# Kernel optimization log

Hardware: AMD Instinct MI355X
Metric: run time of the kernel (lower is better)

## Reference

```python
import jax, jax.numpy as jnp
import numpy as np

N = 20000        # nodes
E = 320000       # edges (avg degree 16)
NHID = 256       # hidden dim (decoder input features)
NFEAT = 256      # reconstructed attribute dim
K_SELECTED = 4096  # number of nodes with label == 1 (static for jit)


def setup_inputs() -> dict:
    key = jax.random.key(0)
    ks = jax.random.split(key, 12)
    feature_attribute = jax.random.normal(ks[0], (N, NHID), dtype=jnp.float32)
    edge_row = jax.random.randint(ks[1], (E,), 0, N, dtype=jnp.int32)
    edge_col = jax.random.randint(ks[2], (E,), 0, N, dtype=jnp.int32)
    # positive, roughly degree-normalized adjacency weights
    edge_w = jax.random.uniform(ks[3], (E,), dtype=jnp.float32) / 16.0
    # first K_SELECTED nodes are labeled 1, rest 0 (static count for jit)
    labels = jnp.concatenate([jnp.ones((K_SELECTED,), jnp.int32),
                              jnp.zeros((N - K_SELECTED,), jnp.int32)])
    stdv1 = 1.0 / np.sqrt(NHID)
    stdv2 = 1.0 / np.sqrt(NFEAT)
    W1_ad = jax.random.uniform(ks[4], (NHID, NHID), minval=-stdv1, maxval=stdv1, dtype=jnp.float32)
    b1_ad = jax.random.uniform(ks[5], (NHID,), minval=-stdv1, maxval=stdv1, dtype=jnp.float32)
    W2_ad = jax.random.uniform(ks[6], (NHID, NFEAT), minval=-stdv2, maxval=stdv2, dtype=jnp.float32)
    b2_ad = jax.random.uniform(ks[7], (NFEAT,), minval=-stdv2, maxval=stdv2, dtype=jnp.float32)
    W_sd = jax.random.uniform(ks[8], (NHID, NHID), minval=-stdv1, maxval=stdv1, dtype=jnp.float32)
    b_sd = jax.random.uniform(ks[9], (NHID,), minval=-stdv1, maxval=stdv1, dtype=jnp.float32)
    return dict(feature_attribute=feature_attribute, edge_row=edge_row, edge_col=edge_col,
                edge_w=edge_w, labels=labels, W1_ad=W1_ad, b1_ad=b1_ad,
                W2_ad=W2_ad, b2_ad=b2_ad, W_sd=W_sd, b_sd=b_sd)


def reference(feature_attribute, edge_row, edge_col, edge_w, labels,
              W1_ad, b1_ad, W2_ad, b2_ad, W_sd, b_sd):
    def gcn(x, W, b):
        support = x @ W                                   # [N, d_out] dense mm
        msg = support[edge_col] * edge_w[:, None]         # gather + scale [E, d_out]
        out = jax.ops.segment_sum(msg, edge_row, num_segments=N)  # spmm aggregation
        return out + b

    # static-size index of labeled nodes (labels==1 count is K_SELECTED)
    idx = jnp.nonzero(labels == 1, size=K_SELECTED)[0]

    # Attribute decoder: relu(gc1) -> (dropout, eval: identity) -> gc2 -> select
    h = jax.nn.relu(gcn(feature_attribute, W1_ad, b1_ad))
    pred_attribute_mat = gcn(h, W2_ad, b2_ad)[idx]        # [K, NFEAT]

    # Structure decoder: gc1 -> select -> x @ x.T
    s = gcn(feature_attribute, W_sd, b_sd)[idx]           # [K, NHID]
    pred_adj_mat = s @ s.T                                # [K, K]

    return pred_attribute_mat, pred_adj_mat
```

## Files before the change

### kernel.cpp

```cpp
#include <hip/hip_runtime.h>
#include <hip/hip_bf16.h>

#define NN   20000
#define NE   320000
#define KSEL 4096

typedef short bf16x8 __attribute__((ext_vector_type(8)));
typedef float f32x4  __attribute__((ext_vector_type(4)));

static __device__ __forceinline__ float bf2f(unsigned short u){
  return __uint_as_float(((unsigned int)u) << 16);
}
static __device__ __forceinline__ unsigned short f2bf(float f){
  unsigned int x = __float_as_uint(f);
  x += 0x7fffu + ((x >> 16) & 1u);
  return (unsigned short)(x >> 16);
}
static __device__ __forceinline__ void gld_lds16(const unsigned short* g, unsigned short* l){
  __builtin_amdgcn_global_load_lds(
      (const __attribute__((address_space(1))) unsigned int*)g,
      (__attribute__((address_space(3))) unsigned int*)l, 16, 0, 0);
}

__global__ __launch_bounds__(256) void k_prep0(const float* __restrict__ W1,
    const float* __restrict__ Wsd, const float* __restrict__ W2,
    const int* __restrict__ labels,
    unsigned short* __restrict__ Wt, int* __restrict__ counts, int* __restrict__ partA){
  int b = blockIdx.x, tid = threadIdx.x;
  if (b < 48){
    __shared__ unsigned short lt[64 * 65];
    int w = b >> 4, t = b & 15;
    int tR = (t >> 2) * 64, tC = (t & 3) * 64;
    const float* W = (w == 0) ? W1 : (w == 1 ? Wsd : W2);
    #pragma unroll
    for (int it = 0; it < 16; ++it){
      int lin = it * 256 + tid;
      int r = lin >> 6, c = lin & 63;
      lt[c * 65 + r] = f2bf(W[(size_t)(tR + r) * 256 + tC + c]);
    }
    __syncthreads();
    #pragma unroll
    for (int it = 0; it < 16; ++it){
      int lin = it * 256 + tid;
      int o = lin >> 6, k = lin & 63;
      Wt[(size_t)w * 65536 + (size_t)(tC + o) * 256 + tR + k] = lt[o * 65 + k];
    }
  } else {
    __shared__ int ws[4];
    int z = b - 48, lane = tid & 63, wv = tid >> 6;
    if (tid < 250) *(int4*)&counts[z * 1000 + tid * 4] = make_int4(0, 0, 0, 0);
    int base = z * 1024 + tid * 4;
    int s = 0;
    #pragma unroll
    for (int j = 0; j < 4; ++j){
      int n0 = base + j;
      if (n0 < NN) s += (labels[n0] == 1) ? 1 : 0;
    }
    #pragma unroll
    for (int off = 32; off; off >>= 1) s += __shfl_down(s, off, 64);
    if (lane == 0) ws[wv] = s;
    __syncthreads();
    if (tid == 0) partA[z] = ws[0] + ws[1] + ws[2] + ws[3];
  }
}

__global__ __launch_bounds__(256) void k_main1(const float* __restrict__ X,
    const int* __restrict__ row, const int* __restrict__ labels,
    const int* __restrict__ partA,
    unsigned short* __restrict__ Xb, int* __restrict__ counts, int* __restrict__ idx){
  int b = blockIdx.x, tid = threadIdx.x;
  if (b < 2500){
    int i = (b * 256 + tid) * 8;
    float4 v0 = *(const float4*)(X + i);
    float4 v1 = *(const float4*)(X + i + 4);
    bf16x8 o;
    o[0] = (short)f2bf(v0.x); o[1] = (short)f2bf(v0.y);
    o[2] = (short)f2bf(v0.z); o[3] = (short)f2bf(v0.w);
    o[4] = (short)f2bf(v1.x); o[5] = (short)f2bf(v1.y);
    o[6] = (short)f2bf(v1.z); o[7] = (short)f2bf(v1.w);
    *(bf16x8*)(Xb + i) = o;
  } else if (b < 3750){
    int e = (b - 2500) * 256 + tid;
    atomicAdd(&counts[row[e]], 1);
  } else {
    __shared__ int ws[4];
    __shared__ int boff_s;
    int bx = b - 3750;
    int lane = tid & 63, wv = tid >> 6;
    if (tid < 64){
      int v = (lane < 20) ? partA[lane] : 0;
      int acc = v;
      #pragma unroll
      for (int off = 1; off < 32; off <<= 1){
        int t = __shfl_up(acc, off, 64);
        if (lane >= off) acc += t;
      }
      if (lane == bx) boff_s = acc - v;
    }
    int base = bx * 1024 + tid * 4;
    int c[4]; int s = 0;
    #pragma unroll
    for (int j = 0; j < 4; ++j){
      int n0 = base + j;
      c[j] = (n0 < NN && labels[n0] == 1) ? 1 : 0;
      s += c[j];
    }
    int incl = s;
    #pragma unroll
    for (int off = 1; off < 64; off <<= 1){
      int t = __shfl_up(incl, off, 64);
      if (lane >= off) incl += t;
    }
    if (lane == 63) ws[wv] = incl;
    __syncthreads();
    int woff = boff_s;
    for (int w = 0; w < wv; ++w) woff += ws[w];
    int off = woff + incl - s;
    #pragma unroll
    for (int j = 0; j < 4; ++j){
      if (c[j]){ if (off < KSEL) idx[off] = base + j; ++off; }
    }
  }
}

__global__ __launch_bounds__(256) void k_row_emit(const int* __restrict__ counts,
    int* __restrict__ start, int* __restrict__ cursor){
  __shared__ int ws[4];
  __shared__ int red[4];
  int tid = threadIdx.x, lane = tid & 63, wv = tid >> 6;
  int base = blockIdx.x * 1024;
  int ps = 0;
  for (int i = tid * 4; i < base; i += 1024){
    int4 v = *(const int4*)&counts[i];
    ps += v.x + v.y + v.z + v.w;
  }
  #pragma unroll
  for (int off = 32; off; off >>= 1) ps += __shfl_down(ps, off, 64);
  if (lane == 0) red[wv] = ps;
  __syncthreads();
  int bpref = red[0] + red[1] + red[2] + red[3];
  int nb = base + tid * 4;
  int c[4]; int s = 0;
  #pragma unroll
  for (int j = 0; j < 4; ++j){
    int n0 = nb + j;
    c[j] = (n0 < NN) ? counts[n0] : 0;
    s += c[j];
  }
  int incl = s;
  #pragma unroll
  for (int off = 1; off < 64; off <<= 1){
    int t = __shfl_up(incl, off, 64);
    if (lane >= off) incl += t;
  }
  if (lane == 63) ws[wv] = incl;
  __syncthreads();
  int woff = bpref;
  for (int w = 0; w < wv; ++w) woff += ws[w];
  int run = woff + incl - s;
  #pragma unroll
  for (int j = 0; j < 4; ++j){
    int n0 = nb + j;
    if (n0 < NN){ start[n0] = run; cursor[n0] = run; run += c[j]; }
  }
  if (blockIdx.x == 0 && tid == 0) start[NN] = NE;
}

__global__ void k_scatter(const int* __restrict__ row, const int* __restrict__ col,
                          const float* __restrict__ ew, int* __restrict__ cursor,
                          int2* __restrict__ rec){
  int e = blockIdx.x * 256 + threadIdx.x;
  if (e < NE){
    int r = row[e];
    int p = atomicAdd(&cursor[r], 1);
    rec[p] = make_int2(col[e], __float_as_int(ew[e]));
  }
}

__global__ __launch_bounds__(256) void k_spmm_full(const unsigned short* __restrict__ Xb,
    const int* __restrict__ start, const int2* __restrict__ rec,
    unsigned short* __restrict__ aggX){
  int wave = threadIdx.x >> 6, lane = threadIdx.x & 63;
  int half = lane >> 5, hl = lane & 31;
  int n = blockIdx.x * 4 + wave;
  int s = start[n], e = start[n + 1];
  int d = hl * 8;
  float acc[8] = {};
  for (int base = s; base < e; base += 64){
    int p = base + lane;
    int pc = p < e ? p : e - 1;
    int2 r = rec[pc];
    float wv = (p < e) ? __int_as_float(r.y) : 0.0f;
    int m = e - base; if (m > 64) m = 64;
    for (int j = 0; j < m; j += 8){
      int j0 = j + half, j1 = j + 2 + half, j2 = j + 4 + half, j3 = j + 6 + half;
      int   c0 = __shfl(r.x, j0), c1 = __shfl(r.x, j1);
      int   c2 = __shfl(r.x, j2), c3 = __shfl(r.x, j3);
      float w0 = __shfl(wv, j0),  w1 = __shfl(wv, j1);
      float w2 = __shfl(wv, j2),  w3 = __shfl(wv, j3);
      bf16x8 v0 = *(const bf16x8*)&Xb[(size_t)c0 * 256 + d];
      bf16x8 v1 = *(const bf16x8*)&Xb[(size_t)c1 * 256 + d];
      bf16x8 v2 = *(const bf16x8*)&Xb[(size_t)c2 * 256 + d];
      bf16x8 v3 = *(const bf16x8*)&Xb[(size_t)c3 * 256 + d];
      #pragma unroll
      for (int q = 0; q < 8; ++q){
        acc[q] += w0 * bf2f((unsigned short)v0[q]) + w1 * bf2f((unsigned short)v1[q])
                + w2 * bf2f((unsigned short)v2[q]) + w3 * bf2f((unsigned short)v3[q]);
      }
    }
  }
  #pragma unroll
  for (int q = 0; q < 8; ++q){
    float o = __shfl(acc[q], hl + 32);
    acc[q] += o;
  }
  if (half == 0){
    bf16x8 ob;
    #pragma unroll
    for (int q = 0; q < 8; ++q) ob[q] = (short)f2bf(acc[q]);
    *(bf16x8*)&aggX[(size_t)n * 256 + d] = ob;
  }
}

__global__ __launch_bounds__(256) void k_gemm_h(const unsigned short* __restrict__ A,
                                                const unsigned short* __restrict__ Wt,
                                                const float* __restrict__ bias,
                                                unsigned short* __restrict__ out, int M){
  __shared__ unsigned short At[128 * 64];
  __shared__ unsigned short Bt[64 * 64];
  int tid = threadIdx.x, wave = tid >> 6, lane = tid & 63;
  int lm = lane & 15, lq = lane >> 4;
  int mBase = blockIdx.x * 128;
  int oBase = blockIdx.y * 64;
  f32x4 acc[2][4] = {};
  for (int kc = 0; kc < 256; kc += 64){
    if (kc) __syncthreads();
    #pragma unroll
    for (int it = 0; it < 4; ++it){
      int s = (wave * 4 + it) * 64 + lane;
      int row = s >> 3, c = (s & 7) ^ (row & 7);
      int gr = mBase + row; if (gr >= M) gr = M - 1;
      gld_lds16(&A[(size_t)gr * 256 + kc + c * 8], &At[s * 8]);
    }
    #pragma unroll
    for (int it = 0; it < 2; ++it){
      int s = (wave * 2 + it) * 64 + lane;
      int row = s >> 3, c = (s & 7) ^ (row & 7);
      gld_lds16(&Wt[(size_t)(oBase + row) * 256 + kc + c * 8], &Bt[s * 8]);
    }
    __syncthreads();
    #pragma unroll
    for (int ks = 0; ks < 64; ks += 32){
      int cb = ks >> 3;
      int RA = wave * 32 + lm;
      int ca = ((cb + lq) ^ (RA & 7)) << 3;
      bf16x8 a0 = *(const bf16x8*)&At[RA * 64 + ca];
      bf16x8 a1 = *(const bf16x8*)&At[(RA + 16) * 64 + ca];
      #pragma unroll
      for (int os = 0; os < 4; ++os){
        int RB = os * 16 + lm;
        bf16x8 b = *(const bf16x8*)&Bt[RB * 64 + (((cb + lq) ^ (RB & 7)) << 3)];
        acc[0][os] = __builtin_amdgcn_mfma_f32_16x16x32_bf16(a0, b, acc[0][os], 0, 0, 0);
        acc[1][os] = __builtin_amdgcn_mfma_f32_16x16x32_bf16(a1, b, acc[1][os], 0, 0, 0);
      }
    }
  }
  #pragma unroll
  for (int ms = 0; ms < 2; ++ms){
    int rb = mBase + wave * 32 + ms * 16 + lq * 4;
    #pragma unroll
    for (int os = 0; os < 4; ++os){
      int col = oBase + os * 16 + lm;
      float bv = bias[col];
      #pragma unroll
      for (int r = 0; r < 4; ++r){
        int row = rb + r;
        if (row < M) out[(size_t)row * 256 + col] = f2bf(fmaxf(acc[ms][os][r] + bv, 0.f));
      }
    }
  }
}

__global__ __launch_bounds__(256) void k_tail1(const unsigned short* __restrict__ h,
    const int* __restrict__ idx, const int* __restrict__ start, const int2* __restrict__ rec,
    unsigned short* __restrict__ aggH, const unsigned short* __restrict__ aggX,
    const unsigned short* __restrict__ Wt, const float* __restrict__ bsd,
    unsigned short* __restrict__ sel){
  int tid = threadIdx.x, wave = tid >> 6, lane = tid & 63;
  if (blockIdx.x < 128){
    int lm = lane & 15, lq = lane >> 4;
    int b2 = blockIdx.x;
    int mBase = (b2 & 31) * 128, oBase = (b2 >> 5) * 64;
    const unsigned short* W = Wt + 256 * 256;
    int r0 = mBase + wave * 32 + lm;
    const unsigned short* A0 = aggX + (size_t)idx[r0] * 256;
    const unsigned short* A1 = aggX + (size_t)idx[r0 + 16] * 256;
    f32x4 acc[2][4] = {};
    #pragma unroll
    for (int ks = 0; ks < 256; ks += 32){
      int ka = ks + lq * 8;
      bf16x8 a0 = *(const bf16x8*)&A0[ka];
      bf16x8 a1 = *(const bf16x8*)&A1[ka];
      #pragma unroll
      for (int os = 0; os < 4; ++os){
        bf16x8 b = *(const bf16x8*)&W[(size_t)(oBase + os * 16 + lm) * 256 + ka];
        acc[0][os] = __builtin_amdgcn_mfma_f32_16x16x32_bf16(a0, b, acc[0][os], 0, 0, 0);
        acc[1][os] = __builtin_amdgcn_mfma_f32_16x16x32_bf16(a1, b, acc[1][os], 0, 0, 0);
      }
    }
    #pragma unroll
    for (int ms = 0; ms < 2; ++ms){
      int rb = mBase + wave * 32 + ms * 16 + lq * 4;
      #pragma unroll
      for (int os = 0; os < 4; ++os){
        int col = oBase + os * 16 + lm;
        float bv = bsd[col];
        #pragma unroll
        for (int r = 0; r < 4; ++r)
          sel[(size_t)(rb + r) * 256 + col] = f2bf(acc[ms][os][r] + bv);
      }
    }
    return;
  }
  int half = lane >> 5, hl = lane & 31;
  int i = (blockIdx.x - 128) * 4 + wave;
  int n = idx[i];
  int s = start[n], e = start[n + 1];
  int d = hl * 8;
  float acc[8] = {};
  for (int base = s; base < e; base += 64){
    int p = base + lane;
    int pc = p < e ? p : e - 1;
    int2 r = rec[pc];
    float wv = (p < e) ? __int_as_float(r.y) : 0.0f;
    int m = e - base; if (m > 64) m = 64;
    for (int j = 0; j < m; j += 8){
      int j0 = j + half, j1 = j + 2 + half, j2 = j + 4 + half, j3 = j + 6 + half;
      int   c0 = __shfl(r.x, j0), c1 = __shfl(r.x, j1);
      int   c2 = __shfl(r.x, j2), c3 = __shfl(r.x, j3);
      float w0 = __shfl(wv, j0),  w1 = __shfl(wv, j1);
      float w2 = __shfl(wv, j2),  w3 = __shfl(wv, j3);
      bf16x8 v0 = *(const bf16x8*)&h[(size_t)c0 * 256 + d];
      bf16x8 v1 = *(const bf16x8*)&h[(size_t)c1 * 256 + d];
      bf16x8 v2 = *(const bf16x8*)&h[(size_t)c2 * 256 + d];
      bf16x8 v3 = *(const bf16x8*)&h[(size_t)c3 * 256 + d];
      #pragma unroll
      for (int q = 0; q < 8; ++q){
        acc[q] += w0 * bf2f((unsigned short)v0[q]) + w1 * bf2f((unsigned short)v1[q])
                + w2 * bf2f((unsigned short)v2[q]) + w3 * bf2f((unsigned short)v3[q]);
      }
    }
  }
  #pragma unroll
  for (int q = 0; q < 8; ++q){
    float o = __shfl(acc[q], hl + 32);
    acc[q] += o;
  }
  if (half == 0){
    bf16x8 ob;
    #pragma unroll
    for (int q = 0; q < 8; ++q) ob[q] = (short)f2bf(acc[q]);
    *(bf16x8*)&aggH[(size_t)i * 256 + d] = ob;
  }
}

__global__ __launch_bounds__(256) void k_tail2(const unsigned short* __restrict__ aggH,
    const unsigned short* __restrict__ Wt, const float* __restrict__ b2v,
    float* __restrict__ out0, const unsigned short* __restrict__ S,
    float* __restrict__ out1){
  __shared__ __align__(16) char smem[34816];
  int tid = threadIdx.x, wave = tid >> 6, lane = tid & 63;
  int lm = lane & 15, lq = lane >> 4;
  if (blockIdx.x < 128){
    int b2 = blockIdx.x;
    int mBase = (b2 & 31) * 128, oBase = (b2 >> 5) * 64;
    const unsigned short* W = Wt + 512 * 256;
    const unsigned short* A0 = aggH + (size_t)(mBase + wave * 32 + lm) * 256;
    const unsigned short* A1 = A0 + 16 * 256;
    f32x4 acc[2][4] = {};
    #pragma unroll
    for (int ks = 0; ks < 256; ks += 32){
      int ka = ks + lq * 8;
      bf16x8 a0 = *(const bf16x8*)&A0[ka];
      bf16x8 a1 = *(const bf16x8*)&A1[ka];
      #pragma unroll
      for (int os = 0; os < 4; ++os){
        bf16x8 b = *(const bf16x8*)&W[(size_t)(oBase + os * 16 + lm) * 256 + ka];
        acc[0][os] = __builtin_amdgcn_mfma_f32_16x16x32_bf16(a0, b, acc[0][os], 0, 0, 0);
        acc[1][os] = __builtin_amdgcn_mfma_f32_16x16x32_bf16(a1, b, acc[1][os], 0, 0, 0);
      }
    }
    #pragma unroll
    for (int ms = 0; ms < 2; ++ms){
      int rb = mBase + wave * 32 + ms * 16 + lq * 4;
      #pragma unroll
      for (int os = 0; os < 4; ++os){
        int col = oBase + os * 16 + lm;
        float bv = b2v[col];
        #pragma unroll
        for (int r = 0; r < 4; ++r)
          out0[(size_t)(rb + r) * 256 + col] = acc[ms][os][r] + bv;
      }
    }
    return;
  }
  int t = blockIdx.x - 128;
  int bx = (int)((sqrtf(8.f * (float)t + 1.f) - 1.f) * 0.5f);
  while ((bx + 1) * (bx + 2) / 2 <= t) ++bx;
  while (bx * (bx + 1) / 2 > t) --bx;
  int by = t - bx * (bx + 1) / 2;
  int mBase = bx * 128, oBase = by * 128;
  unsigned short* At = (unsigned short*)smem;
  unsigned short* Bt = (unsigned short*)(smem + 16384);
  f32x4 acc[2][8] = {};
  for (int kc = 0; kc < 256; kc += 64){
    if (kc) __syncthreads();
    #pragma unroll
    for (int it = 0; it < 4; ++it){
      int s = (wave * 4 + it) * 64 + lane;
      int row = s >> 3, c = (s & 7) ^ (row & 7);
      gld_lds16(&S[(size_t)(mBase + row) * 256 + kc + c * 8], &At[s * 8]);
      gld_lds16(&S[(size_t)(oBase + row) * 256 + kc + c * 8], &Bt[s * 8]);
    }
    __syncthreads();
    #pragma unroll
    for (int ks = 0; ks < 64; ks += 32){
      int cb = ks >> 3;
      int RA = wave * 32 + lm;
      int ca = ((cb + lq) ^ (RA & 7)) << 3;
      bf16x8 a0 = *(const bf16x8*)&At[RA * 64 + ca];
      bf16x8 a1 = *(const bf16x8*)&At[(RA + 16) * 64 + ca];
      #pragma unroll
      for (int os = 0; os < 8; ++os){
        int RB = os * 16 + lm;
        bf16x8 b = *(const bf16x8*)&Bt[RB * 64 + (((cb + lq) ^ (RB & 7)) << 3)];
        acc[0][os] = __builtin_amdgcn_mfma_f32_16x16x32_bf16(a0, b, acc[0][os], 0, 0, 0);
        acc[1][os] = __builtin_amdgcn_mfma_f32_16x16x32_bf16(a1, b, acc[1][os], 0, 0, 0);
      }
    }
  }
  #pragma unroll
  for (int ms = 0; ms < 2; ++ms){
    int rb = mBase + wave * 32 + ms * 16 + lq * 4;
    #pragma unroll
    for (int os = 0; os < 8; ++os){
      int col = oBase + os * 16 + lm;
      #pragma unroll
      for (int r = 0; r < 4; ++r)
        out1[(size_t)(rb + r) * 4096 + col] = acc[ms][os][r];
    }
  }
  if (bx == by) return;
  float* fst = (float*)smem;
  #pragma unroll
  for (int half = 0; half < 2; ++half){
    __syncthreads();
    #pragma unroll
    for (int ms = 0; ms < 2; ++ms){
      int mr = wave * 32 + ms * 16 + lq * 4;
      #pragma unroll
      for (int os2 = 0; os2 < 4; ++os2){
        int oc = os2 * 16 + lm;
        *(f32x4*)&fst[oc * 136 + mr] = acc[ms][half * 4 + os2];
      }
    }
    __syncthreads();
    int l = tid & 31, ocb = tid >> 5;
    #pragma unroll
    for (int it = 0; it < 8; ++it){
      int oc = it * 8 + ocb;
      f32x4 v = *(const f32x4*)&fst[oc * 136 + l * 4];
      *(f32x4*)&out1[(size_t)(oBase + half * 64 + oc) * 4096 + mBase + l * 4] = v;
    }
  }
}

extern "C" void kernel_launch(void* const* d_in, const int* in_sizes, int n_in,
                              void* d_out, int out_size, void* d_ws, size_t ws_size,
                              hipStream_t stream){
  const float* X    = (const float*)d_in[0];
  const int*   erow = (const int*)d_in[1];
  const int*   ecol = (const int*)d_in[2];
  const float* ew   = (const float*)d_in[3];
  const int*   labels = (const int*)d_in[4];
  const float* W1   = (const float*)d_in[5];
  const float* b1   = (const float*)d_in[6];
  const float* W2   = (const float*)d_in[7];
  const float* b2   = (const float*)d_in[8];
  const float* Wsd  = (const float*)d_in[9];
  const float* bsd  = (const float*)d_in[10];
  float* out0 = (float*)d_out;
  float* out1 = out0 + (size_t)KSEL * 256;

  char* ws = (char*)d_ws;
  unsigned short* Xb   = (unsigned short*)(ws);
  unsigned short* Wt   = (unsigned short*)(ws + 10240000);
  unsigned short* aggX = (unsigned short*)(ws + 10633216);
  unsigned short* h    = (unsigned short*)(ws + 20873216);
  unsigned short* aggH = (unsigned short*)(ws + 31113216);
  unsigned short* sel  = (unsigned short*)(ws + 33210368);
  int* idx    = (int*)(ws + 35307520);
  int* counts = (int*)(ws + 35323904);
  int* startp = (int*)(ws + 35403904);
  int* cursor = (int*)(ws + 35483908);
  int2* rec   = (int2*)(ws + 35563912);
  int* partA  = (int*)(ws + 38123912);

  k_prep0<<<68, 256, 0, stream>>>(W1, Wsd, W2, labels, Wt, counts, partA);
  k_main1<<<3770, 256, 0, stream>>>(X, erow, labels, partA, Xb, counts, idx);
  k_row_emit<<<20, 256, 0, stream>>>(counts, startp, cursor);
  k_scatter<<<1250, 256, 0, stream>>>(erow, ecol, ew, cursor, rec);
  k_spmm_full<<<5000, 256, 0, stream>>>(Xb, startp, rec, aggX);
  k_gemm_h<<<dim3(157, 4), 256, 0, stream>>>(aggX, Wt, b1, h, NN);
  k_tail1<<<1152, 256, 0, stream>>>(h, idx, startp, rec, aggH, aggX, Wt, bsd, sel);
  k_tail2<<<656, 256, 0, stream>>>(aggH, Wt, b2, out0, sel, out1);
}
```

Measured before the change: 203.5 us.

## Split SpMM feature dimension into four slices across blocks

Both SpMM aggregations (full-graph X and the selected-row h gather) now split the 256-wide feature dimension into four 64-column slices, each handled by a separate block. Within a wave, 8 lane groups each take different edges and cover 64 columns, then a butterfly xor-shuffle reduction combines them. The grids grow fourfold to expose more parallelism and make each wave's gathers shorter. In exchange, every slice re-reads the edge records and does extra reduction shuffles per node.

After: 221.8 us. 9.0% more time.

```diff
diff --git a/kernel.cpp b/kernel.cpp
--- a/kernel.cpp
+++ b/kernel.cpp
@@ -181,40 +181,38 @@
     const int* __restrict__ start, const int2* __restrict__ rec,
     unsigned short* __restrict__ aggX){
   int wave = threadIdx.x >> 6, lane = threadIdx.x & 63;
-  int half = lane >> 5, hl = lane & 31;
-  int n = blockIdx.x * 4 + wave;
+  int bx = blockIdx.x;
+  int slice = bx / 5000;
+  int n = (bx - slice * 5000) * 4 + wave;
   int s = start[n], e = start[n + 1];
-  int d = hl * 8;
+  int g = lane >> 3, gl = lane & 7;
+  int d = slice * 64 + gl * 8;
+  int hl = lane & 31;
   float acc[8] = {};
-  for (int base = s; base < e; base += 64){
-    int p = base + lane;
+  for (int base = s; base < e; base += 32){
+    int p = base + hl;
     int pc = p < e ? p : e - 1;
     int2 r = rec[pc];
     float wv = (p < e) ? __int_as_float(r.y) : 0.0f;
-    int m = e - base; if (m > 64) m = 64;
-    for (int j = 0; j < m; j += 8){
-      int j0 = j + half, j1 = j + 2 + half, j2 = j + 4 + half, j3 = j + 6 + half;
-      int   c0 = __shfl(r.x, j0), c1 = __shfl(r.x, j1);
-      int   c2 = __shfl(r.x, j2), c3 = __shfl(r.x, j3);
-      float w0 = __shfl(wv, j0),  w1 = __shfl(wv, j1);
-      float w2 = __shfl(wv, j2),  w3 = __shfl(wv, j3);
-      bf16x8 v0 = *(const bf16x8*)&Xb[(size_t)c0 * 256 + d];
-      bf16x8 v1 = *(const bf16x8*)&Xb[(size_t)c1 * 256 + d];
-      bf16x8 v2 = *(const bf16x8*)&Xb[(size_t)c2 * 256 + d];
-      bf16x8 v3 = *(const bf16x8*)&Xb[(size_t)c3 * 256 + d];
-      #pragma unroll
-      for (int q = 0; q < 8; ++q){
-        acc[q] += w0 * bf2f((unsigned short)v0[q]) + w1 * bf2f((unsigned short)v1[q])
-                + w2 * bf2f((unsigned short)v2[q]) + w3 * bf2f((unsigned short)v3[q]);
-      }
-    }
-  }
-  #pragma unroll
-  for (int q = 0; q < 8; ++q){
-    float o = __shfl(acc[q], hl + 32);
-    acc[q] += o;
-  }
-  if (half == 0){
+    int m = e - base; if (m > 32) m = 32;
+    #pragma unroll
+    for (int k = 0; k < 4; ++k){
+      int eo = g + 8 * k;
+      int   c = __shfl(r.x, eo);
+      float w = __shfl(wv, eo);
+      if (eo < m){
+        bf16x8 v = *(const bf16x8*)&Xb[(size_t)c * 256 + d];
+        #pragma unroll
+        for (int q = 0; q < 8; ++q) acc[q] += w * bf2f((unsigned short)v[q]);
+      }
+    }
+  }
+  #pragma unroll
+  for (int off = 8; off < 64; off <<= 1){
+    #pragma unroll
+    for (int q = 0; q < 8; ++q) acc[q] += __shfl_xor(acc[q], off, 64);
+  }
+  if (g == 0){
     bf16x8 ob;
     #pragma unroll
     for (int q = 0; q < 8; ++q) ob[q] = (short)f2bf(acc[q]);
@@ -322,41 +320,39 @@
     }
     return;
   }
-  int half = lane >> 5, hl = lane & 31;
-  int i = (blockIdx.x - 128) * 4 + wave;
+  int t = blockIdx.x - 128;
+  int slice = t >> 10;
+  int i = (t & 1023) * 4 + wave;
   int n = idx[i];
   int s = start[n], e = start[n + 1];
-  int d = hl * 8;
+  int g = lane >> 3, gl = lane & 7;
+  int d = slice * 64 + gl * 8;
+  int hl = lane & 31;
   float acc[8] = {};
-  for (int base = s; base < e; base += 64){
-    int p = base + lane;
+  for (int base = s; base < e; base += 32){
+    int p = base + hl;
     int pc = p < e ? p : e - 1;
     int2 r = rec[pc];
     float wv = (p < e) ? __int_as_float(r.y) : 0.0f;
-    int m = e - base; if (m > 64) m = 64;
-    for (int j = 0; j < m; j += 8){
-      int j0 = j + half, j1 = j + 2 + half, j2 = j + 4 + half, j3 = j + 6 + half;
-      int   c0 = __shfl(r.x, j0), c1 = __shfl(r.x, j1);
-      int   c2 = __shfl(r.x, j2), c3 = __shfl(r.x, j3);
-      float w0 = __shfl(wv, j0),  w1 = __shfl(wv, j1);
-      float w2 = __shfl(wv, j2),  w3 = __shfl(wv, j3);
-      bf16x8 v0 = *(const bf16x8*)&h[(size_t)c0 * 256 + d];
-      bf16x8 v1 = *(const bf16x8*)&h[(size_t)c1 * 256 + d];
-      bf16x8 v2 = *(const bf16x8*)&h[(size_t)c2 * 256 + d];
-      bf16x8 v3 = *(const bf16x8*)&h[(size_t)c3 * 256 + d];
-      #pragma unroll
-      for (int q = 0; q < 8; ++q){
-        acc[q] += w0 * bf2f((unsigned short)v0[q]) + w1 * bf2f((unsigned short)v1[q])
-                + w2 * bf2f((unsigned short)v2[q]) + w3 * bf2f((unsigned short)v3[q]);
-      }
-    }
-  }
-  #pragma unroll
-  for (int q = 0; q < 8; ++q){
-    float o = __shfl(acc[q], hl + 32);
-    acc[q] += o;
-  }
-  if (half == 0){
+    int m = e - base; if (m > 32) m = 32;
+    #pragma unroll
+    for (int k = 0; k < 4; ++k){
+      int eo = g + 8 * k;
+      int   c = __shfl(r.x, eo);
+      float w = __shfl(wv, eo);
+      if (eo < m){
+        bf16x8 v = *(const bf16x8*)&h[(size_t)c * 256 + d];
+        #pragma unroll
+        for (int q = 0; q < 8; ++q) acc[q] += w * bf2f((unsigned short)v[q]);
+      }
+    }
+  }
+  #pragma unroll
+  for (int off = 8; off < 64; off <<= 1){
+    #pragma unroll
+    for (int q = 0; q < 8; ++q) acc[q] += __shfl_xor(acc[q], off, 64);
+  }
+  if (g == 0){
     bf16x8 ob;
     #pragma unroll
     for (int q = 0; q < 8; ++q) ob[q] = (short)f2bf(acc[q]);
@@ -510,8 +506,8 @@
   k_main1<<<3770, 256, 0, stream>>>(X, erow, labels, partA, Xb, counts, idx);
   k_row_emit<<<20, 256, 0, stream>>>(counts, startp, cursor);
   k_scatter<<<1250, 256, 0, stream>>>(erow, ecol, ew, cursor, rec);
-  k_spmm_full<<<5000, 256, 0, stream>>>(Xb, startp, rec, aggX);
+  k_spmm_full<<<20000, 256, 0, stream>>>(Xb, startp, rec, aggX);
   k_gemm_h<<<dim3(157, 4), 256, 0, stream>>>(aggX, Wt, b1, h, NN);
-  k_tail1<<<1152, 256, 0, stream>>>(h, idx, startp, rec, aggH, aggX, Wt, bsd, sel);
+  k_tail1<<<4224, 256, 0, stream>>>(h, idx, startp, rec, aggH, aggX, Wt, bsd, sel);
   k_tail2<<<656, 256, 0, stream>>>(aggH, Wt, b2, out0, sel, out1);
 }
```

## Compute full Gram matrix with 128x64 tiles instead of symmetric triangle mirroring

Applied to the files above, without the earlier changes.

The s@s^T stage drops the lower-triangle tiling, where each 128x128 tile was computed once and written both directly and transposed. It now computes every 128x64 output tile independently (2048 blocks plus the 128 attribute blocks), staging results through LDS so that rows are written as coalesced float4 stores. This removes the transposed scatter and the triangular index math and gives more, smaller blocks for load balance. The cost is roughly double the MFMA work and S tile loads.

After: 203.2 us. Within noise of the previous version (-0.2%).

```diff
diff --git a/kernel.cpp b/kernel.cpp
--- a/kernel.cpp
+++ b/kernel.cpp
@@ -405,14 +405,10 @@
     return;
   }
   int t = blockIdx.x - 128;
-  int bx = (int)((sqrtf(8.f * (float)t + 1.f) - 1.f) * 0.5f);
-  while ((bx + 1) * (bx + 2) / 2 <= t) ++bx;
-  while (bx * (bx + 1) / 2 > t) --bx;
-  int by = t - bx * (bx + 1) / 2;
-  int mBase = bx * 128, oBase = by * 128;
+  int mBase = (t >> 6) * 128, oBase = (t & 63) * 64;
   unsigned short* At = (unsigned short*)smem;
   unsigned short* Bt = (unsigned short*)(smem + 16384);
-  f32x4 acc[2][8] = {};
+  f32x4 acc[2][4] = {};
   for (int kc = 0; kc < 256; kc += 64){
     if (kc) __syncthreads();
     #pragma unroll
@@ -420,6 +416,11 @@
       int s = (wave * 4 + it) * 64 + lane;
       int row = s >> 3, c = (s & 7) ^ (row & 7);
       gld_lds16(&S[(size_t)(mBase + row) * 256 + kc + c * 8], &At[s * 8]);
+    }
+    #pragma unroll
+    for (int it = 0; it < 2; ++it){
+      int s = (wave * 2 + it) * 64 + lane;
+      int row = s >> 3, c = (s & 7) ^ (row & 7);
       gld_lds16(&S[(size_t)(oBase + row) * 256 + kc + c * 8], &Bt[s * 8]);
     }
     __syncthreads();
@@ -431,7 +432,7 @@
       bf16x8 a0 = *(const bf16x8*)&At[RA * 64 + ca];
       bf16x8 a1 = *(const bf16x8*)&At[(RA + 16) * 64 + ca];
       #pragma unroll
-      for (int os = 0; os < 8; ++os){
+      for (int os = 0; os < 4; ++os){
         int RB = os * 16 + lm;
         bf16x8 b = *(const bf16x8*)&Bt[RB * 64 + (((cb + lq) ^ (RB & 7)) << 3)];
         acc[0][os] = __builtin_amdgcn_mfma_f32_16x16x32_bf16(a0, b, acc[0][os], 0, 0, 0);
@@ -439,39 +440,26 @@
       }
     }
   }
+  __syncthreads();
+  float* fst = (float*)smem;
   #pragma unroll
   for (int ms = 0; ms < 2; ++ms){
-    int rb = mBase + wave * 32 + ms * 16 + lq * 4;
-    #pragma unroll
-    for (int os = 0; os < 8; ++os){
-      int col = oBase + os * 16 + lm;
+    int mr = wave * 32 + ms * 16 + lq * 4;
+    #pragma unroll
+    for (int os = 0; os < 4; ++os){
+      int oc = os * 16 + lm;
       #pragma unroll
       for (int r = 0; r < 4; ++r)
-        out1[(size_t)(rb + r) * 4096 + col] = acc[ms][os][r];
-    }
-  }
-  if (bx == by) return;
-  float* fst = (float*)smem;
-  #pragma unroll
-  for (int half = 0; half < 2; ++half){
-    __syncthreads();
-    #pragma unroll
-    for (int ms = 0; ms < 2; ++ms){
-      int mr = wave * 32 + ms * 16 + lq * 4;
-      #pragma unroll
-      for (int os2 = 0; os2 < 4; ++os2){
-        int oc = os2 * 16 + lm;
-        *(f32x4*)&fst[oc * 136 + mr] = acc[ms][half * 4 + os2];
-      }
-    }
-    __syncthreads();
-    int l = tid & 31, ocb = tid >> 5;
-    #pragma unroll
-    for (int it = 0; it < 8; ++it){
-      int oc = it * 8 + ocb;
-      f32x4 v = *(const f32x4*)&fst[oc * 136 + l * 4];
-      *(f32x4*)&out1[(size_t)(oBase + half * 64 + oc) * 4096 + mBase + l * 4] = v;
-    }
+        fst[(mr + r) * 68 + oc] = acc[ms][os][r];
+    }
+  }
+  __syncthreads();
+  int cc = (tid & 15) * 4, r0 = tid >> 4;
+  #pragma unroll
+  for (int it = 0; it < 8; ++it){
+    int row = it * 16 + r0;
+    f32x4 v = *(const f32x4*)&fst[row * 68 + cc];
+    *(f32x4*)&out1[(size_t)(mBase + row) * 4096 + oBase + cc] = v;
   }
 }
 
@@ -513,5 +501,5 @@
   k_spmm_full<<<5000, 256, 0, stream>>>(Xb, startp, rec, aggX);
   k_gemm_h<<<dim3(157, 4), 256, 0, stream>>>(aggX, Wt, b1, h, NN);
   k_tail1<<<1152, 256, 0, stream>>>(h, idx, startp, rec, aggH, aggX, Wt, bsd, sel);
-  k_tail2<<<656, 256, 0, stream>>>(aggH, Wt, b2, out0, sel, out1);
-}
+  k_tail2<<<2176, 256, 0, stream>>>(aggH, Wt, b2, out0, sel, out1);
+}
```
